# Kernel optimization log

Measured on AMD Instinct MI355X. Metric: run time of the kernel, lower is better.

Reference implementation:

```python
import jax, jax.numpy as jnp
import numpy as np

K = 2  # kernel_size == stride (required by the module's output view)


def setup_inputs() -> dict:
    key = jax.random.key(0)
    k1, k2, k3, k4, k5 = jax.random.split(key, 5)
    b, c, h, w = 16, 64, 224, 224
    x = jax.random.normal(k1, (b, c, h, w), dtype=jnp.float32)
    # torch nn.Linear params: W1 [16, K*K], b1 [16], W2 [1, 16], b2 [1]
    s1 = 1.0 / np.sqrt(K * K)
    s2 = 1.0 / np.sqrt(16)
    W1 = jax.random.uniform(k2, (16, K * K), jnp.float32, -s1, s1)
    b1 = jax.random.uniform(k3, (16,), jnp.float32, -s1, s1)
    W2 = jax.random.uniform(k4, (1, 16), jnp.float32, -s2, s2)
    b2 = jax.random.uniform(k5, (1,), jnp.float32, -s2, s2)
    return {"x": x, "W1": W1, "b1": b1, "W2": W2, "b2": b2}


def reference(x, W1, b1, W2, b2):
    b, c, h, w = x.shape
    nh, nw = h // K, w // K
    # non-overlapping KxK patches, flattened row-major within patch
    # (matches torch unfold(2,K,K).unfold(3,K,K).view(..., K*K))
    patches = x.reshape(b, c, nh, K, nw, K)
    patches = patches.transpose(0, 1, 2, 4, 3, 5).reshape(b, c, nh, nw, K * K)
    # tiny MLP per patch: K*K -> 16 -> 1
    hdn = jax.nn.relu(jnp.einsum('bcijk,hk->bcijh', patches, W1) + b1)
    out = jnp.einsum('bcijh,oh->bcijo', hdn, W2) + b2
    return out[..., 0]  # [b, c, h//K, w//K]
```

## Files before the change

kernel.cpp:

```cpp
#include <hip/hip_runtime.h>


#define NJ 56

__global__ __launch_bounds__(256)
void nn_pool_kernel(const float* __restrict__ x,
                    const float* __restrict__ W1,
                    const float* __restrict__ b1,
                    const float* __restrict__ W2,
                    const float* __restrict__ b2,
                    float* __restrict__ out,
                    int n_units)
{
    const int tid = blockIdx.x * 256 + threadIdx.x;
    if (tid >= n_units) return;

    const int j = tid % NJ;
    const int r = tid / NJ;

    const float* p0 = x + (size_t)r * 448 + j * 4;
    const float4 t0 = *reinterpret_cast<const float4*>(p0);
    const float4 t1 = *reinterpret_cast<const float4*>(p0 + 224);

    float w0[16], w1[16], w2c[16], w3[16], bb[16], v2[16];
#pragma unroll
    for (int h = 0; h < 16; ++h) {
        w0[h]  = W1[4 * h + 0];
        w1[h]  = W1[4 * h + 1];
        w2c[h] = W1[4 * h + 2];
        w3[h]  = W1[4 * h + 3];
        bb[h]  = b1[h];
        v2[h]  = W2[h];
    }
    const float c2 = b2[0];

    float aA = c2, aB = c2;
#pragma unroll
    for (int h = 0; h < 16; ++h) {
        float sA = fmaf(w0[h], t0.x, bb[h]);
        float sB = fmaf(w0[h], t0.z, bb[h]);
        sA = fmaf(w1[h], t0.y, sA);
        sB = fmaf(w1[h], t0.w, sB);
        sA = fmaf(w2c[h], t1.x, sA);
        sB = fmaf(w2c[h], t1.z, sB);
        sA = fmaf(w3[h], t1.y, sA);
        sB = fmaf(w3[h], t1.w, sB);
        aA = fmaf(v2[h], fmaxf(sA, 0.0f), aA);
        aB = fmaf(v2[h], fmaxf(sB, 0.0f), aB);
    }

    float2 res;
    res.x = aA;
    res.y = aB;
    *reinterpret_cast<float2*>(out + (size_t)r * 112 + j * 2) = res;
}

extern "C" void kernel_launch(void* const* d_in, const int* in_sizes, int n_in,
                              void* d_out, int out_size, void* d_ws, size_t ws_size,
                              hipStream_t stream) {
    const float* x  = (const float*)d_in[0];
    const float* W1 = (const float*)d_in[1];
    const float* b1 = (const float*)d_in[2];
    const float* W2 = (const float*)d_in[3];
    const float* b2 = (const float*)d_in[4];
    float* out = (float*)d_out;

    const int n_units = out_size / 2;
    const int block = 256;
    const int grid = (n_units + block - 1) / block;
    nn_pool_kernel<<<grid, block, 0, stream>>>(x, W1, b1, W2, b2, out, n_units);
}
```

Before: 290.4 us.

## Process four outputs per thread with packed FP32 v2 FMA math

Each thread now computes four pooled outputs instead of two. It loads four float4 values and writes one float4. The MLP math is expressed with 2-wide float vectors so the compiler can emit packed FMA/max instructions, and the bounds check and 64-bit index math are dropped. The aim is to halve per-output instruction count and widen memory accesses. The trade-offs are that it relies on out_size dividing exactly by 1024 and on 32-bit offsets fitting in int, and it launches half as many threads.

After: 294.6 us. No clear change (+1.4%).

```diff
diff --git a/kernel.cpp b/kernel.cpp
--- a/kernel.cpp
+++ b/kernel.cpp
@@ -1,7 +1,9 @@
 #include <hip/hip_runtime.h>
 
 
-#define NJ 56
+typedef float v2f __attribute__((ext_vector_type(2)));
+
+#define NJ4 28
 
 __global__ __launch_bounds__(256)
 void nn_pool_kernel(const float* __restrict__ x,
@@ -9,50 +11,53 @@
                     const float* __restrict__ b1,
                     const float* __restrict__ W2,
                     const float* __restrict__ b2,
-                    float* __restrict__ out,
-                    int n_units)
+                    float* __restrict__ out)
 {
     const int tid = blockIdx.x * 256 + threadIdx.x;
-    if (tid >= n_units) return;
+    const int j = tid % NJ4;
+    const int r = tid / NJ4;
 
-    const int j = tid % NJ;
-    const int r = tid / NJ;
+    const float* p0 = x + r * 448 + j * 8;
+    const float4 r0a = *reinterpret_cast<const float4*>(p0);
+    const float4 r0b = *reinterpret_cast<const float4*>(p0 + 4);
+    const float4 r1a = *reinterpret_cast<const float4*>(p0 + 224);
+    const float4 r1b = *reinterpret_cast<const float4*>(p0 + 228);
 
-    const float* p0 = x + (size_t)r * 448 + j * 4;
-    const float4 t0 = *reinterpret_cast<const float4*>(p0);
-    const float4 t1 = *reinterpret_cast<const float4*>(p0 + 224);
+    const float c2 = b2[0];
 
-    float w0[16], w1[16], w2c[16], w3[16], bb[16], v2[16];
+    const v2f a0 = {r0a.x, r0a.z}, a1 = {r0a.y, r0a.w};
+    const v2f a2 = {r1a.x, r1a.z}, a3 = {r1a.y, r1a.w};
+    const v2f c0 = {r0b.x, r0b.z}, c1 = {r0b.y, r0b.w};
+    const v2f c2v = {r1b.x, r1b.z}, c3 = {r1b.y, r1b.w};
+
+    v2f accA = {c2, c2}, accB = {c2, c2};
 #pragma unroll
     for (int h = 0; h < 16; ++h) {
-        w0[h]  = W1[4 * h + 0];
-        w1[h]  = W1[4 * h + 1];
-        w2c[h] = W1[4 * h + 2];
-        w3[h]  = W1[4 * h + 3];
-        bb[h]  = b1[h];
-        v2[h]  = W2[h];
-    }
-    const float c2 = b2[0];
+        const float w0 = W1[4 * h + 0];
+        const float w1 = W1[4 * h + 1];
+        const float w2 = W1[4 * h + 2];
+        const float w3 = W1[4 * h + 3];
+        const float bb = b1[h];
+        const float vv = W2[h];
 
-    float aA = c2, aB = c2;
-#pragma unroll
-    for (int h = 0; h < 16; ++h) {
-        float sA = fmaf(w0[h], t0.x, bb[h]);
-        float sB = fmaf(w0[h], t0.z, bb[h]);
-        sA = fmaf(w1[h], t0.y, sA);
-        sB = fmaf(w1[h], t0.w, sB);
-        sA = fmaf(w2c[h], t1.x, sA);
-        sB = fmaf(w2c[h], t1.z, sB);
-        sA = fmaf(w3[h], t1.y, sA);
-        sB = fmaf(w3[h], t1.w, sB);
-        aA = fmaf(v2[h], fmaxf(sA, 0.0f), aA);
-        aB = fmaf(v2[h], fmaxf(sB, 0.0f), aB);
+        v2f sA = {bb, bb}, sB = {bb, bb};
+        sA = __builtin_elementwise_fma(a0, (v2f){w0, w0}, sA);
+        sB = __builtin_elementwise_fma(c0, (v2f){w0, w0}, sB);
+        sA = __builtin_elementwise_fma(a1, (v2f){w1, w1}, sA);
+        sB = __builtin_elementwise_fma(c1, (v2f){w1, w1}, sB);
+        sA = __builtin_elementwise_fma(a2, (v2f){w2, w2}, sA);
+        sB = __builtin_elementwise_fma(c2v, (v2f){w2, w2}, sB);
+        sA = __builtin_elementwise_fma(a3, (v2f){w3, w3}, sA);
+        sB = __builtin_elementwise_fma(c3, (v2f){w3, w3}, sB);
+        sA = __builtin_elementwise_max(sA, (v2f){0.f, 0.f});
+        sB = __builtin_elementwise_max(sB, (v2f){0.f, 0.f});
+        accA = __builtin_elementwise_fma(sA, (v2f){vv, vv}, accA);
+        accB = __builtin_elementwise_fma(sB, (v2f){vv, vv}, accB);
     }
 
-    float2 res;
-    res.x = aA;
-    res.y = aB;
-    *reinterpret_cast<float2*>(out + (size_t)r * 112 + j * 2) = res;
+    float4 res;
+    res.x = accA.x; res.y = accA.y; res.z = accB.x; res.w = accB.y;
+    *reinterpret_cast<float4*>(out + r * 112 + j * 4) = res;
 }
 
 extern "C" void kernel_launch(void* const* d_in, const int* in_sizes, int n_in,
@@ -65,8 +70,8 @@
     const float* b2 = (const float*)d_in[4];
     float* out = (float*)d_out;
 
-    const int n_units = out_size / 2;
+    const int n_quads = out_size / 4;
     const int block = 256;
-    const int grid = (n_units + block - 1) / block;
-    nn_pool_kernel<<<grid, block, 0, stream>>>(x, W1, b1, W2, b2, out, n_units);
+    const int grid = n_quads / block;
+    nn_pool_kernel<<<grid, block, 0, stream>>>(x, W1, b1, W2, b2, out);
 }
```
